# Performance work log

Hardware: AMD Instinct MI355X
Metric: run time of the kernel (lower is better)

## Reference

```python
import jax, jax.numpy as jnp
import numpy as np

B, T, C, H = 8, 2048, 1024, 64

def setup_inputs() -> dict:
    key = jax.random.key(0)
    k1, k2, k3, k4 = jax.random.split(key, 4)
    return {
        "inputs": jax.random.normal(k1, (B, T, C), dtype=jnp.float32),
        "Wq": jax.random.normal(k2, (C, H), dtype=jnp.float32) * (C ** -0.5),
        "Wk": jax.random.normal(k3, (C, H), dtype=jnp.float32) * (C ** -0.5),
        "Wv": jax.random.normal(k4, (C, H), dtype=jnp.float32) * (C ** -0.5),
    }

def reference(inputs, Wq, Wk, Wv):
    # q,k,v: [B,T,H]
    q = jnp.einsum('btc,ch->bth', inputs, Wq)
    k = jnp.einsum('btc,ch->bth', inputs, Wk)
    v = jnp.einsum('btc,ch->bth', inputs, Wv)
    c = inputs.shape[-1]
    # NOTE: original scales by C**-0.5 (embedding dim), not head_size**-0.5
    scale = jnp.asarray(c, inputs.dtype) ** -0.5
    wei = jnp.einsum('bqh,bkh->bqk', q, k) * scale  # [B,T,T]
    t = inputs.shape[1]
    causal = jnp.tril(jnp.ones((t, t), dtype=bool))
    wei = jnp.where(causal[None, :, :], wei, -jnp.inf)
    wei = jax.nn.softmax(wei, axis=-1)
    # dropout is identity in eval / DROP_RATE=0
    out = jnp.einsum('bqk,bkh->bqh', wei, v)  # [B,T,H]
    return out
```

## Files before the change

kernel.cpp:

```cpp
#include <hip/hip_runtime.h>
#include <stdint.h>

#define B_ 8
#define T_ 2048
#define C_ 1024
#define H_ 64
#define M_ (B_*T_)

typedef __bf16 bf16x8 __attribute__((ext_vector_type(8)));
typedef float  f32x4  __attribute__((ext_vector_type(4)));

union U4B { uint4 u; bf16x8 v; };

__device__ __forceinline__ unsigned short f32_to_bf16(float f) {
    union { float f; uint32_t u; } c; c.f = f;
    uint32_t u = c.u;
    u += 0x7fffu + ((u >> 16) & 1u);
    return (unsigned short)(u >> 16);
}
__device__ __forceinline__ uint32_t pack2_bf16(float a, float b) {
#if __has_builtin(__builtin_amdgcn_cvt_pk_bf16_f32)
    typedef __bf16 bf16x2 __attribute__((ext_vector_type(2)));
    union { bf16x2 v; uint32_t u; } c;
    c.v = __builtin_amdgcn_cvt_pk_bf16_f32(a, b);
    return c.u;
#else
    return (uint32_t)f32_to_bf16(a) | ((uint32_t)f32_to_bf16(b) << 16);
#endif
}

__global__ __launch_bounds__(256) void prepack_w(const float* __restrict__ Wq,
        const float* __restrict__ Wk, const float* __restrict__ Wv,
        unsigned short* __restrict__ wpk) {
    int o = blockIdx.x * 256 + threadIdx.x;
    if (o >= 24576) return;
    int lane = o & 63, nt = (o >> 6) % 12, kc = o / (64 * 12);
    int l15 = lane & 15, grp = lane >> 4;
    int n = nt * 16 + l15;
    int k = kc * 32 + grp * 8;
    const float* W = (n < 64) ? Wq : (n < 128) ? Wk : Wv;
    int col = n & 63;
    unsigned short tmp[8];
    #pragma unroll
    for (int j = 0; j < 8; j++) tmp[j] = f32_to_bf16(W[(size_t)(k + j) * 64 + col]);
    *(uint4*)(wpk + (size_t)o * 8) = *(uint4*)tmp;
}

__global__ __launch_bounds__(256, 4) void qkv_kernel(const float* __restrict__ X,
        const unsigned short* __restrict__ wpk,
        unsigned short* __restrict__ qb, unsigned short* __restrict__ kb,
        unsigned short* __restrict__ vt) {
    __shared__ unsigned short Xl[2][16 * 512];
    const int tid = threadIdx.x;
    const int wave = tid >> 6, lane = tid & 63;
    const int grp = lane >> 4, l15 = lane & 15;
    const int h = wave;
    const int t16 = blockIdx.x;

    const int rr = tid >> 4, ch = tid & 15;
    const float* xrow = X + ((size_t)t16 * 16 + rr) * 1024 + ch * 8;
    const int swzst = (rr & 7) << 4;
    const unsigned short* wp = wpk + ((size_t)(h * 3) * 64 + lane) * 8;
    const int xswz = (l15 & 7) << 4;

#define STAGE_LOAD(la, lb, hh)                                                 \
    _Pragma("unroll")                                                          \
    for (int i = 0; i < 4; i++) {                                              \
        la[i] = *(const float4*)(xrow + (hh) * 512 + i * 128);                 \
        lb[i] = *(const float4*)(xrow + (hh) * 512 + i * 128 + 4);             \
    }

#define STAGE_WRITE(la, lb, hh)                                                \
    {                                                                          \
        char* xd = (char*)&Xl[hh][0] + rr * 1024;                              \
        _Pragma("unroll")                                                      \
        for (int i = 0; i < 4; i++) {                                          \
            uint4 pk = (uint4){ pack2_bf16(la[i].x, la[i].y),                  \
                                pack2_bf16(la[i].z, la[i].w),                  \
                                pack2_bf16(lb[i].x, lb[i].y),                  \
                                pack2_bf16(lb[i].z, lb[i].w) };                \
            *(uint4*)(xd + ((ch * 16 + i * 256) ^ swzst)) = pk;                \
        }                                                                      \
    }

#define COMPUTE_HALF(h2)                                                       \
    {                                                                          \
        const char* xs = (const char*)&Xl[h2][0] + l15 * 1024;                 \
        U4B xr0, xr1, xr2;                                                     \
        xr0.u = *(const uint4*)(xs + ((0 * 64 + grp * 16) ^ xswz));            \
        xr1.u = *(const uint4*)(xs + ((1 * 64 + grp * 16) ^ xswz));            \
        xr2.u = *(const uint4*)(xs + ((2 * 64 + grp * 16) ^ xswz));            \
        _Pragma("unroll")                                                      \
        for (int kcl = 0; kcl < 16; kcl++) {                                   \
            const int kcg = (h2) * 16 + kcl;                                   \
            const int q = kcl & 3;                                             \
            U4B a = (kcl % 3 == 0) ? xr0 : (kcl % 3 == 1) ? xr1 : xr2;         \
            U4B b0, b1, b2;                                                    \
            b0.u = w[q][0]; b1.u = w[q][1]; b2.u = w[q][2];                    \
            acc[0] = __builtin_amdgcn_mfma_f32_16x16x32_bf16(a.v, b0.v, acc[0], 0, 0, 0); \
            acc[1] = __builtin_amdgcn_mfma_f32_16x16x32_bf16(a.v, b1.v, acc[1], 0, 0, 0); \
            acc[2] = __builtin_amdgcn_mfma_f32_16x16x32_bf16(a.v, b2.v, acc[2], 0, 0, 0); \
            if (kcl + 3 < 16) {                                                \
                U4B t;                                                         \
                t.u = *(const uint4*)(xs + (((kcl + 3) * 64 + grp * 16) ^ xswz)); \
                if (kcl % 3 == 0) xr0 = t; else if (kcl % 3 == 1) xr1 = t; else xr2 = t; \
            }                                                                  \
            if (kcg + 4 < 32) {                                                \
                const unsigned short* wn = wp + ((size_t)(kcg + 4) * 768) * 8; \
                _Pragma("unroll")                                              \
                for (int jj = 0; jj < 3; jj++)                                 \
                    w[q][jj] = *(const uint4*)(wn + jj * 64 * 8);              \
            }                                                                  \
        }                                                                      \
    }

    f32x4 acc[3];
    #pragma unroll
    for (int j = 0; j < 3; j++) acc[j] = (f32x4){0.f, 0.f, 0.f, 0.f};

    float4 xa[4], xb[4], ya[4], yb[4];
    STAGE_LOAD(xa, xb, 0)
    uint4 w[4][3];
    #pragma unroll
    for (int d = 0; d < 4; d++)
        #pragma unroll
        for (int jj = 0; jj < 3; jj++)
            w[d][jj] = *(const uint4*)(wp + ((size_t)(d * 768 + jj * 64)) * 8);
    STAGE_LOAD(ya, yb, 1)
    STAGE_WRITE(xa, xb, 0)
    asm volatile("s_waitcnt lgkmcnt(0)" ::: "memory");
    __builtin_amdgcn_s_barrier();

    COMPUTE_HALF(0)

    STAGE_WRITE(ya, yb, 1)
    asm volatile("s_waitcnt lgkmcnt(0)" ::: "memory");
    __builtin_amdgcn_s_barrier();

    COMPUTE_HALF(1)

#undef STAGE_LOAD
#undef STAGE_WRITE
#undef COMPUTE_HALF

    const int r0 = t16 * 16 + grp * 4;
    const int bb = r0 >> 11;
    const int t0 = r0 & 2047;
    #pragma unroll
    for (int jj = 0; jj < 3; jj++) {
        int col = (h * 3 + jj) * 16 + l15;
        if (col < 64) {
            for (int r = 0; r < 4; r++)
                qb[(size_t)(r0 + r) * 64 + col] = f32_to_bf16(acc[jj][r] * 0.03125f);
        } else if (col < 128) {
            for (int r = 0; r < 4; r++)
                kb[(size_t)(r0 + r) * 64 + (col - 64)] = f32_to_bf16(acc[jj][r]);
        } else {
            int c = col - 128;
            ushort4 vv;
            vv.x = f32_to_bf16(acc[jj][0]); vv.y = f32_to_bf16(acc[jj][1]);
            vv.z = f32_to_bf16(acc[jj][2]); vv.w = f32_to_bf16(acc[jj][3]);
            *(ushort4*)(vt + ((size_t)bb * 64 + c) * 2048 + t0) = vv;
        }
    }
}

__global__ __launch_bounds__(256) void attn1_kernel(const unsigned short* __restrict__ qb,
        const unsigned short* __restrict__ kb, const unsigned short* __restrict__ vt,
        float* __restrict__ pl, float* __restrict__ pacc) {
    __shared__ unsigned short Kl[64][72];
    __shared__ unsigned short Vl[64][72];
    const int tid = threadIdx.x;
    const int wave = tid >> 6, lane = tid & 63;
    const int grp = lane >> 4, l15 = lane & 15;
    const int b = blockIdx.x & 7;
    int f = blockIdx.x >> 3;
    int g = 0;
    for (; g < 32; g++) { int c = (35 - g) >> 2; if (f < c) break; f -= c; }
    const int j = 31 - g;
    const int s = f;
    const int ktend = min(4, (j + 1) - 4 * s);
    const int qbase = j * 64 + wave * 16;

    const unsigned short* qp = qb + ((size_t)b * 2048 + qbase + l15) * 64 + grp * 8;
    bf16x8 bq0 = *(const bf16x8*)qp;
    bf16x8 bq1 = *(const bf16x8*)(qp + 32);

    float lsum = 0.f;
    f32x4 acc[4];
    for (int d = 0; d < 4; d++) acc[d] = (f32x4){0.f, 0.f, 0.f, 0.f};

    const unsigned short* kB = kb + ((size_t)b * 2048 + s * 256) * 64;
    const unsigned short* vB = vt + (size_t)b * 64 * 2048 + s * 256;
    const int r1 = tid >> 3, c1 = (tid & 7) * 8;
    const int r2 = (tid + 256) >> 3, c2 = c1;

    uint4 kr0, kr1, vr0, vr1;
    kr0 = *(const uint4*)(kB + (size_t)r1 * 64 + c1);
    kr1 = *(const uint4*)(kB + (size_t)r2 * 64 + c2);
    vr0 = *(const uint4*)(vB + (size_t)r1 * 2048 + c1);
    vr1 = *(const uint4*)(vB + (size_t)r2 * 2048 + c2);

    for (int kt = 0; kt < ktend; kt++) {
        *(uint4*)&Kl[r1][c1] = kr0;  *(uint4*)&Kl[r2][c2] = kr1;
        *(uint4*)&Vl[r1][c1] = vr0;  *(uint4*)&Vl[r2][c2] = vr1;
        __syncthreads();
        if (kt + 1 < ktend) {
            const unsigned short* kN = kB + (size_t)(kt + 1) * 64 * 64;
            const unsigned short* vN = vB + (kt + 1) * 64;
            kr0 = *(const uint4*)(kN + (size_t)r1 * 64 + c1);
            kr1 = *(const uint4*)(kN + (size_t)r2 * 64 + c2);
            vr0 = *(const uint4*)(vN + (size_t)r1 * 2048 + c1);
            vr1 = *(const uint4*)(vN + (size_t)r2 * 2048 + c2);
        }
        const int keybase = s * 256 + kt * 64;
        f32x4 st[4];
        #pragma unroll
        for (int nt = 0; nt < 4; nt++) {
            bf16x8 a0 = *(const bf16x8*)&Kl[nt * 16 + l15][grp * 8];
            bf16x8 a1 = *(const bf16x8*)&Kl[nt * 16 + l15][32 + grp * 8];
            f32x4 t = (f32x4){0.f, 0.f, 0.f, 0.f};
            t = __builtin_amdgcn_mfma_f32_16x16x32_bf16(a0, bq0, t, 0, 0, 0);
            t = __builtin_amdgcn_mfma_f32_16x16x32_bf16(a1, bq1, t, 0, 0, 0);
            st[nt] = t;
        }
        if (keybase + 63 > qbase) {
            int q = qbase + l15;
            #pragma unroll
            for (int nt = 0; nt < 4; nt++)
                for (int r = 0; r < 4; r++)
                    if (keybase + nt * 16 + grp * 4 + r > q) st[nt][r] = -1e30f;
        }
        float p[4][4];
        #pragma unroll
        for (int nt = 0; nt < 4; nt++)
            for (int r = 0; r < 4; r++) { p[nt][r] = __expf(st[nt][r]); lsum += p[nt][r]; }
        uint32_t t0a = pack2_bf16(p[0][0], p[0][1]), t0b = pack2_bf16(p[0][2], p[0][3]);
        uint32_t t1a = pack2_bf16(p[1][0], p[1][1]), t1b = pack2_bf16(p[1][2], p[1][3]);
        uint32_t t2a = pack2_bf16(p[2][0], p[2][1]), t2b = pack2_bf16(p[2][2], p[2][3]);
        uint32_t t3a = pack2_bf16(p[3][0], p[3][1]), t3b = pack2_bf16(p[3][2], p[3][3]);
        const int s0l = ((grp & 1) << 5) + l15, s1l = s0l + 16;
        const bool hi = (grp >= 2);
        U4B bw0, bw1;
        {
            uint32_t e0a = (uint32_t)__shfl((int)t0a, s0l, 64);
            uint32_t e0b = (uint32_t)__shfl((int)t0b, s0l, 64);
            uint32_t e0c = (uint32_t)__shfl((int)t0a, s1l, 64);
            uint32_t e0d = (uint32_t)__shfl((int)t0b, s1l, 64);
            uint32_t e1a = (uint32_t)__shfl((int)t1a, s0l, 64);
            uint32_t e1b = (uint32_t)__shfl((int)t1b, s0l, 64);
            uint32_t e1c = (uint32_t)__shfl((int)t1a, s1l, 64);
            uint32_t e1d = (uint32_t)__shfl((int)t1b, s1l, 64);
            bw0.u = (uint4){ hi ? e1a : e0a, hi ? e1b : e0b, hi ? e1c : e0c, hi ? e1d : e0d };
        }
        {
            uint32_t e0a = (uint32_t)__shfl((int)t2a, s0l, 64);
            uint32_t e0b = (uint32_t)__shfl((int)t2b, s0l, 64);
            uint32_t e0c = (uint32_t)__shfl((int)t2a, s1l, 64);
            uint32_t e0d = (uint32_t)__shfl((int)t2b, s1l, 64);
            uint32_t e1a = (uint32_t)__shfl((int)t3a, s0l, 64);
            uint32_t e1b = (uint32_t)__shfl((int)t3b, s0l, 64);
            uint32_t e1c = (uint32_t)__shfl((int)t3a, s1l, 64);
            uint32_t e1d = (uint32_t)__shfl((int)t3b, s1l, 64);
            bw1.u = (uint4){ hi ? e1a : e0a, hi ? e1b : e0b, hi ? e1c : e0c, hi ? e1d : e0d };
        }
        #pragma unroll
        for (int dt = 0; dt < 4; dt++) {
            bf16x8 av0 = *(const bf16x8*)&Vl[dt * 16 + l15][grp * 8];
            bf16x8 av1 = *(const bf16x8*)&Vl[dt * 16 + l15][32 + grp * 8];
            acc[dt] = __builtin_amdgcn_mfma_f32_16x16x32_bf16(av0, bw0.v, acc[dt], 0, 0, 0);
            acc[dt] = __builtin_amdgcn_mfma_f32_16x16x32_bf16(av1, bw1.v, acc[dt], 0, 0, 0);
        }
        __syncthreads();
    }
    lsum += __shfl_xor(lsum, 16, 64);
    lsum += __shfl_xor(lsum, 32, 64);
    size_t rowq = (size_t)b * 2048 + qbase + l15;
    size_t p = rowq * 8 + s;
    if (grp == 0) pl[p] = lsum;
    #pragma unroll
    for (int dt = 0; dt < 4; dt++)
        *(f32x4*)&pacc[p * 64 + dt * 16 + grp * 4] = acc[dt];
}

__global__ __launch_bounds__(256) void attn2_kernel(const float* __restrict__ pl,
        const float* __restrict__ pacc, float* __restrict__ out) {
    int idx = blockIdx.x * 256 + threadIdx.x;
    int row = idx >> 4;
    int d0 = (idx & 15) * 4;
    int t = row & 2047;
    int ns = ((t >> 6) + 4) >> 2;
    float den = 0.f;
    f32x4 num = (f32x4){0.f, 0.f, 0.f, 0.f};
    for (int s = 0; s < ns; s++) {
        den += pl[(size_t)row * 8 + s];
        num += *(const f32x4*)&pacc[((size_t)row * 8 + s) * 64 + d0];
    }
    float inv = 1.f / den;
    *(f32x4*)&out[(size_t)row * 64 + d0] = num * inv;
}

extern "C" void kernel_launch(void* const* d_in, const int* in_sizes, int n_in,
                              void* d_out, int out_size, void* d_ws, size_t ws_size,
                              hipStream_t stream) {
    const float* X  = (const float*)d_in[0];
    const float* Wq = (const float*)d_in[1];
    const float* Wk = (const float*)d_in[2];
    const float* Wv = (const float*)d_in[3];
    float* out = (float*)d_out;

    unsigned short* qb  = (unsigned short*)d_ws;
    unsigned short* kb  = qb + (size_t)M_ * 64;
    unsigned short* wpk = kb + (size_t)M_ * 64;
    unsigned short* vt  = wpk + (size_t)24576 * 8;
    float* pl   = (float*)(vt + (size_t)B_ * 64 * 2048);
    float* pacc = pl + (size_t)M_ * 8;

    prepack_w<<<96, 256, 0, stream>>>(Wq, Wk, Wv, wpk);
    qkv_kernel<<<1024, 256, 0, stream>>>(X, wpk, qb, kb, vt);
    attn1_kernel<<<1152, 256, 0, stream>>>(qb, kb, vt, pl, pacc);
    attn2_kernel<<<1024, 256, 0, stream>>>(pl, pacc, out);
}
```

Before: 134.5 us.

## Enlarge QKV projection tile to 64 rows per block for weight reuse

The QKV projection kernel now handles 64 token rows per block instead of 16, with four M sub-tiles per wave, so each weight fragment loaded from global memory feeds four times as many MFMAs. The grid shrinks from 1024 to 256 blocks, and the staging buffer grows to 64x512 bf16 (64 KB) with no double-buffering across halves. X loads are no longer overlapped with the first half's compute, and the higher register and LDS use reduces occupancy. With only 256 blocks there may be too little parallelism to fill all CUs.

```diff
diff --git a/kernel.cpp b/kernel.cpp
--- a/kernel.cpp
+++ b/kernel.cpp
@@ -46,67 +46,87 @@
     *(uint4*)(wpk + (size_t)o * 8) = *(uint4*)tmp;
 }
 
-__global__ __launch_bounds__(256, 4) void qkv_kernel(const float* __restrict__ X,
+__global__ __launch_bounds__(256) void qkv_kernel(const float* __restrict__ X,
         const unsigned short* __restrict__ wpk,
         unsigned short* __restrict__ qb, unsigned short* __restrict__ kb,
         unsigned short* __restrict__ vt) {
-    __shared__ unsigned short Xl[2][16 * 512];
+    __shared__ unsigned short Xl[64 * 512];
     const int tid = threadIdx.x;
     const int wave = tid >> 6, lane = tid & 63;
     const int grp = lane >> 4, l15 = lane & 15;
     const int h = wave;
-    const int t16 = blockIdx.x;
+    const int t64 = blockIdx.x;
 
     const int rr = tid >> 4, ch = tid & 15;
-    const float* xrow = X + ((size_t)t16 * 16 + rr) * 1024 + ch * 8;
     const int swzst = (rr & 7) << 4;
     const unsigned short* wp = wpk + ((size_t)(h * 3) * 64 + lane) * 8;
     const int xswz = (l15 & 7) << 4;
 
-#define STAGE_LOAD(la, lb, hh)                                                 \
+    f32x4 acc[4][3];
+    #pragma unroll
+    for (int m = 0; m < 4; m++)
+        #pragma unroll
+        for (int j = 0; j < 3; j++) acc[m][j] = (f32x4){0.f, 0.f, 0.f, 0.f};
+
+    uint4 w[4][3];
+
+#define STAGE_HALF(hh)                                                         \
     _Pragma("unroll")                                                          \
-    for (int i = 0; i < 4; i++) {                                              \
-        la[i] = *(const float4*)(xrow + (hh) * 512 + i * 128);                 \
-        lb[i] = *(const float4*)(xrow + (hh) * 512 + i * 128 + 4);             \
-    }
-
-#define STAGE_WRITE(la, lb, hh)                                                \
-    {                                                                          \
-        char* xd = (char*)&Xl[hh][0] + rr * 1024;                              \
+    for (int s = 0; s < 4; s++) {                                              \
+        const float* xrow = X + ((size_t)t64 * 64 + s * 16 + rr) * 1024        \
+                              + (hh) * 512 + ch * 8;                           \
+        float4 xa[4], xb[4];                                                   \
         _Pragma("unroll")                                                      \
         for (int i = 0; i < 4; i++) {                                          \
-            uint4 pk = (uint4){ pack2_bf16(la[i].x, la[i].y),                  \
-                                pack2_bf16(la[i].z, la[i].w),                  \
-                                pack2_bf16(lb[i].x, lb[i].y),                  \
-                                pack2_bf16(lb[i].z, lb[i].w) };                \
+            xa[i] = *(const float4*)(xrow + i * 128);                          \
+            xb[i] = *(const float4*)(xrow + i * 128 + 4);                      \
+        }                                                                      \
+        char* xd = (char*)Xl + (s * 16 + rr) * 1024;                           \
+        _Pragma("unroll")                                                      \
+        for (int i = 0; i < 4; i++) {                                          \
+            uint4 pk = (uint4){ pack2_bf16(xa[i].x, xa[i].y),                  \
+                                pack2_bf16(xa[i].z, xa[i].w),                  \
+                                pack2_bf16(xb[i].x, xb[i].y),                  \
+                                pack2_bf16(xb[i].z, xb[i].w) };                \
             *(uint4*)(xd + ((ch * 16 + i * 256) ^ swzst)) = pk;                \
         }                                                                      \
     }
 
-#define COMPUTE_HALF(h2)                                                       \
+#define WRING_PROLOGUE(hh)                                                     \
+    _Pragma("unroll")                                                          \
+    for (int d = 0; d < 4; d++)                                                \
+        _Pragma("unroll")                                                      \
+        for (int jj = 0; jj < 3; jj++)                                         \
+            w[d][jj] = *(const uint4*)(wp + (size_t)(((hh) * 16 + d) * 768 + jj * 64) * 8);
+
+#define COMPUTE_HALF(hh)                                                       \
     {                                                                          \
-        const char* xs = (const char*)&Xl[h2][0] + l15 * 1024;                 \
-        U4B xr0, xr1, xr2;                                                     \
-        xr0.u = *(const uint4*)(xs + ((0 * 64 + grp * 16) ^ xswz));            \
-        xr1.u = *(const uint4*)(xs + ((1 * 64 + grp * 16) ^ xswz));            \
-        xr2.u = *(const uint4*)(xs + ((2 * 64 + grp * 16) ^ xswz));            \
+        U4B ar[2][4];                                                          \
+        _Pragma("unroll")                                                      \
+        for (int m = 0; m < 4; m++)                                            \
+            ar[0][m].u = *(const uint4*)((const char*)Xl + (m * 16 + l15) * 1024 \
+                                         + ((grp * 16) ^ xswz));               \
         _Pragma("unroll")                                                      \
         for (int kcl = 0; kcl < 16; kcl++) {                                   \
-            const int kcg = (h2) * 16 + kcl;                                   \
+            const int cur = kcl & 1, nxt = cur ^ 1;                            \
+            if (kcl < 15) {                                                    \
+                _Pragma("unroll")                                              \
+                for (int m = 0; m < 4; m++)                                    \
+                    ar[nxt][m].u = *(const uint4*)((const char*)Xl             \
+                        + (m * 16 + l15) * 1024                                \
+                        + (((kcl + 1) * 64 + grp * 16) ^ xswz));               \
+            }                                                                  \
             const int q = kcl & 3;                                             \
-            U4B a = (kcl % 3 == 0) ? xr0 : (kcl % 3 == 1) ? xr1 : xr2;         \
             U4B b0, b1, b2;                                                    \
             b0.u = w[q][0]; b1.u = w[q][1]; b2.u = w[q][2];                    \
-            acc[0] = __builtin_amdgcn_mfma_f32_16x16x32_bf16(a.v, b0.v, acc[0], 0, 0, 0); \
-            acc[1] = __builtin_amdgcn_mfma_f32_16x16x32_bf16(a.v, b1.v, acc[1], 0, 0, 0); \
-            acc[2] = __builtin_amdgcn_mfma_f32_16x16x32_bf16(a.v, b2.v, acc[2], 0, 0, 0); \
-            if (kcl + 3 < 16) {                                                \
-                U4B t;                                                         \
-                t.u = *(const uint4*)(xs + (((kcl + 3) * 64 + grp * 16) ^ xswz)); \
-                if (kcl % 3 == 0) xr0 = t; else if (kcl % 3 == 1) xr1 = t; else xr2 = t; \
+            _Pragma("unroll")                                                  \
+            for (int m = 0; m < 4; m++) {                                      \
+                acc[m][0] = __builtin_amdgcn_mfma_f32_16x16x32_bf16(ar[cur][m].v, b0.v, acc[m][0], 0, 0, 0); \
+                acc[m][1] = __builtin_amdgcn_mfma_f32_16x16x32_bf16(ar[cur][m].v, b1.v, acc[m][1], 0, 0, 0); \
+                acc[m][2] = __builtin_amdgcn_mfma_f32_16x16x32_bf16(ar[cur][m].v, b2.v, acc[m][2], 0, 0, 0); \
             }                                                                  \
-            if (kcg + 4 < 32) {                                                \
-                const unsigned short* wn = wp + ((size_t)(kcg + 4) * 768) * 8; \
+            if (kcl + 4 < 16) {                                                \
+                const unsigned short* wn = wp + (size_t)(((hh) * 16 + kcl + 4) * 768) * 8; \
                 _Pragma("unroll")                                              \
                 for (int jj = 0; jj < 3; jj++)                                 \
                     w[q][jj] = *(const uint4*)(wn + jj * 64 * 8);              \
@@ -114,53 +134,41 @@
         }                                                                      \
     }
 
-    f32x4 acc[3];
+    STAGE_HALF(0)
+    WRING_PROLOGUE(0)
+    __syncthreads();
+    COMPUTE_HALF(0)
+    __syncthreads();
+    STAGE_HALF(1)
+    WRING_PROLOGUE(1)
+    __syncthreads();
+    COMPUTE_HALF(1)
+
+#undef STAGE_HALF
+#undef WRING_PROLOGUE
+#undef COMPUTE_HALF
+
     #pragma unroll
-    for (int j = 0; j < 3; j++) acc[j] = (f32x4){0.f, 0.f, 0.f, 0.f};
-
-    float4 xa[4], xb[4], ya[4], yb[4];
-    STAGE_LOAD(xa, xb, 0)
-    uint4 w[4][3];
-    #pragma unroll
-    for (int d = 0; d < 4; d++)
-        #pragma unroll
-        for (int jj = 0; jj < 3; jj++)
-            w[d][jj] = *(const uint4*)(wp + ((size_t)(d * 768 + jj * 64)) * 8);
-    STAGE_LOAD(ya, yb, 1)
-    STAGE_WRITE(xa, xb, 0)
-    asm volatile("s_waitcnt lgkmcnt(0)" ::: "memory");
-    __builtin_amdgcn_s_barrier();
-
-    COMPUTE_HALF(0)
-
-    STAGE_WRITE(ya, yb, 1)
-    asm volatile("s_waitcnt lgkmcnt(0)" ::: "memory");
-    __builtin_amdgcn_s_barrier();
-
-    COMPUTE_HALF(1)
-
-#undef STAGE_LOAD
-#undef STAGE_WRITE
-#undef COMPUTE_HALF
-
-    const int r0 = t16 * 16 + grp * 4;
-    const int bb = r0 >> 11;
-    const int t0 = r0 & 2047;
-    #pragma unroll
-    for (int jj = 0; jj < 3; jj++) {
-        int col = (h * 3 + jj) * 16 + l15;
-        if (col < 64) {
-            for (int r = 0; r < 4; r++)
-                qb[(size_t)(r0 + r) * 64 + col] = f32_to_bf16(acc[jj][r] * 0.03125f);
-        } else if (col < 128) {
-            for (int r = 0; r < 4; r++)
-                kb[(size_t)(r0 + r) * 64 + (col - 64)] = f32_to_bf16(acc[jj][r]);
-        } else {
-            int c = col - 128;
-            ushort4 vv;
-            vv.x = f32_to_bf16(acc[jj][0]); vv.y = f32_to_bf16(acc[jj][1]);
-            vv.z = f32_to_bf16(acc[jj][2]); vv.w = f32_to_bf16(acc[jj][3]);
-            *(ushort4*)(vt + ((size_t)bb * 64 + c) * 2048 + t0) = vv;
+    for (int m = 0; m < 4; m++) {
+        const int r0 = t64 * 64 + m * 16 + grp * 4;
+        const int bb = r0 >> 11;
+        const int t0 = r0 & 2047;
+        #pragma unroll
+        for (int jj = 0; jj < 3; jj++) {
+            int col = (h * 3 + jj) * 16 + l15;
+            if (col < 64) {
+                for (int r = 0; r < 4; r++)
+                    qb[(size_t)(r0 + r) * 64 + col] = f32_to_bf16(acc[m][jj][r] * 0.03125f);
+            } else if (col < 128) {
+                for (int r = 0; r < 4; r++)
+                    kb[(size_t)(r0 + r) * 64 + (col - 64)] = f32_to_bf16(acc[m][jj][r]);
+            } else {
+                int c = col - 128;
+                ushort4 vv;
+                vv.x = f32_to_bf16(acc[m][jj][0]); vv.y = f32_to_bf16(acc[m][jj][1]);
+                vv.z = f32_to_bf16(acc[m][jj][2]); vv.w = f32_to_bf16(acc[m][jj][3]);
+                *(ushort4*)(vt + ((size_t)bb * 64 + c) * 2048 + t0) = vv;
+            }
         }
     }
 }
@@ -317,7 +325,7 @@
     float* pacc = pl + (size_t)M_ * 8;
 
     prepack_w<<<96, 256, 0, stream>>>(Wq, Wk, Wv, wpk);
-    qkv_kernel<<<1024, 256, 0, stream>>>(X, wpk, qb, kb, vt);
+    qkv_kernel<<<256, 256, 0, stream>>>(X, wpk, qb, kb, vt);
     attn1_kernel<<<1152, 256, 0, stream>>>(qb, kb, vt, pl, pacc);
     attn2_kernel<<<1024, 256, 0, stream>>>(pl, pacc, out);
 }
```

Measured after the change: 128.5 us. 1.05x faster.
